# Kernel tuning notes

Hardware: AMD Instinct MI355X
Metric: run time of the kernel (lower is better)

The kernel has to match this reference:

```python
import jax, jax.numpy as jnp
import numpy as np

N_EMB = 1024
N_HEAD = 16
HD = N_EMB // N_HEAD
ROPE_BASE = 10000.0


def _rope_cos_sin(seq_len, dim, dtype):
    inv_freq = 1.0 / (ROPE_BASE ** (jnp.arange(0, dim, 2, dtype=jnp.float32) / dim))
    t = jnp.arange(seq_len, dtype=jnp.float32)
    freqs = jnp.outer(t, inv_freq)              # [S, dim/2]
    emb = jnp.concatenate([freqs, freqs], -1)    # [S, dim]
    return jnp.cos(emb).astype(dtype), jnp.sin(emb).astype(dtype)


def _rotate_half(x):
    x1, x2 = jnp.split(x, 2, axis=-1)
    return jnp.concatenate([-x2, x1], axis=-1)


def _apply_rope(x):
    # x: [B, H, L, hd]; rotary over sequence axis (-2)
    cos, sin = _rope_cos_sin(x.shape[-2], x.shape[-1], x.dtype)
    return x * cos + _rotate_half(x) * sin


def setup_inputs() -> dict:
    key = jax.random.key(0)
    ks = jax.random.split(key, 8)
    B, T, S = 2, 2048, 2048
    std = 0.02
    return {
        "x": jax.random.normal(ks[0], (B, T, N_EMB), jnp.float32),
        "memory": jax.random.normal(ks[1], (B, S, N_EMB), jnp.float32),
        "q_w": jax.random.normal(ks[2], (N_EMB, N_EMB), jnp.float32) * std,
        "q_b": jnp.zeros((N_EMB,), jnp.float32),
        "kv_w": jax.random.normal(ks[3], (N_EMB, 2 * N_EMB), jnp.float32) * std,
        "kv_b": jnp.zeros((2 * N_EMB,), jnp.float32),
        "proj_w": jax.random.normal(ks[4], (N_EMB, N_EMB), jnp.float32) * std,
        "proj_b": jnp.zeros((N_EMB,), jnp.float32),
    }


def reference(x, memory, q_w, q_b, kv_w, kv_b, proj_w, proj_b):
    B, S, C = memory.shape
    T = x.shape[1]
    kv = memory @ kv_w + kv_b                      # [B,S,2C]
    K, V = jnp.split(kv, 2, axis=-1)
    Q = x @ q_w + q_b                              # [B,T,C]

    def heads(t, L):
        return t.reshape(B, L, N_HEAD, HD).transpose(0, 2, 1, 3)

    Q, K, V = heads(Q, T), heads(K, S), heads(V, S)
    Q = jax.nn.elu(Q) + 1.0                        # positive feature map
    K = jax.nn.elu(K) + 1.0
    Q_rot = _apply_rope(Q)
    K_rot = _apply_rope(K)
    # denom row-sum: sum_s Q.K_s == Q . (sum_s K_s) -- identical math, no SxT matrix
    denom = jnp.einsum('bhtd,bhd->bht', Q, K.sum(axis=2))[..., None]  # [B,H,T,1]
    att = jnp.einsum('bhtd,bhsd->bhts', Q_rot, K_rot) / denom          # [B,H,T,S]
    y = jnp.einsum('bhts,bhsd->bhtd', att, V)                          # [B,H,T,hd]
    y = y.transpose(0, 2, 1, 3).reshape(B, T, C)
    return y @ proj_w + proj_b
```

## Files before the change

### kernel.cpp

```cpp
#include <hip/hip_runtime.h>
#include <cstddef>
#include <cstdint>

#define B_SZ  2
#define T_SEQ 2048
#define S_SEQ 2048
#define C_EMB 1024
#define NH    16
#define HD    64
#define KDIM  1024

typedef __attribute__((ext_vector_type(8))) short bf16x8;
typedef __attribute__((ext_vector_type(4))) float f32x4;

#define OFF_XH    ((size_t)0)
#define OFF_XL    ((size_t)2097152)
#define OFF_MEMH  ((size_t)4194304)
#define OFF_MEML  ((size_t)6291456)
#define OFF_QWH   ((size_t)8388608)
#define OFF_QWL   ((size_t)8912896)
#define OFF_KVWH  ((size_t)9437184)
#define OFF_KVWL  ((size_t)10485760)
#define OFF_PWH   ((size_t)11534336)
#define OFF_PWL   ((size_t)12058624)
#define OFF_KSUM  ((size_t)12582912)
#define OFF_MT    ((size_t)12584960)
#define OFF_TAB   ((size_t)12716032)
#define OFF_YH    ((size_t)12847104)
#define OFF_YL    ((size_t)14944256)
#define WS_FLOATS ((size_t)17041408)

__device__ __forceinline__ float elu1(float v) {
    return v > 0.0f ? v + 1.0f : __expf(v);
}
__device__ __forceinline__ unsigned short bf16_rne(float x) {
    union { float f; unsigned int u; } v; v.f = x;
    unsigned int u = v.u;
    return (unsigned short)((u + 0x7FFFu + ((u >> 16) & 1u)) >> 16);
}
__device__ __forceinline__ float bf16_to_f(unsigned short h) {
    union { unsigned int u; float f; } v; v.u = ((unsigned int)h) << 16;
    return v.f;
}

#define PREP_BLOCKS 13064

__device__ __forceinline__ void split4_body(
    const float4* __restrict__ in, ushort4* __restrict__ hi,
    ushort4* __restrict__ lo, int i)
{
    float4 v = in[i];
    ushort4 h, l;
    h.x = bf16_rne(v.x); l.x = bf16_rne(v.x - bf16_to_f(h.x));
    h.y = bf16_rne(v.y); l.y = bf16_rne(v.y - bf16_to_f(h.y));
    h.z = bf16_rne(v.z); l.z = bf16_rne(v.z - bf16_to_f(h.z));
    h.w = bf16_rne(v.w); l.w = bf16_rne(v.w - bf16_to_f(h.w));
    hi[i] = h; lo[i] = l;
}

__device__ __forceinline__ void transpose_body(
    const float* __restrict__ W, unsigned short* __restrict__ Wth,
    unsigned short* __restrict__ Wtl, int K, int N, int bx, int by,
    float (*tile)[33])
{
    const int k0 = by * 32, n0 = bx * 32;
    const int tx = threadIdx.x & 31, ty = threadIdx.x >> 5;
    #pragma unroll
    for (int j = 0; j < 4; ++j)
        tile[ty + j * 8][tx] = W[(size_t)(k0 + ty + j * 8) * N + n0 + tx];
    __syncthreads();
    #pragma unroll
    for (int j = 0; j < 4; ++j) {
        float x = tile[tx][ty + j * 8];
        unsigned short h = bf16_rne(x);
        unsigned short l = bf16_rne(x - bf16_to_f(h));
        size_t o = (size_t)(n0 + ty + j * 8) * K + k0 + tx;
        Wth[o] = h; Wtl[o] = l;
    }
}

__global__ __launch_bounds__(256) void prep_kernel(
    const float* __restrict__ x, const float* __restrict__ memory,
    const float* __restrict__ q_w, const float* __restrict__ kv_w,
    const float* __restrict__ proj_w,
    unsigned short* __restrict__ xh, unsigned short* __restrict__ xl,
    unsigned short* __restrict__ mh, unsigned short* __restrict__ ml,
    unsigned short* __restrict__ qwh, unsigned short* __restrict__ qwl,
    unsigned short* __restrict__ kvwh, unsigned short* __restrict__ kvwl,
    unsigned short* __restrict__ pwh, unsigned short* __restrict__ pwl,
    float2* __restrict__ tab, float* __restrict__ zero_base)
{
    __shared__ float tile[32][33];
    const int bid = blockIdx.x;
    const int tid = threadIdx.x;
    if (bid < 4096) {
        split4_body((const float4*)x, (ushort4*)xh, (ushort4*)xl, bid * 256 + tid);
    } else if (bid < 8192) {
        split4_body((const float4*)memory, (ushort4*)mh, (ushort4*)ml, (bid - 4096) * 256 + tid);
    } else if (bid < 9216) {
        int i = bid - 8192;
        transpose_body(q_w, qwh, qwl, 1024, 1024, i & 31, i >> 5, tile);
    } else if (bid < 11264) {
        int i = bid - 9216;
        transpose_body(kv_w, kvwh, kvwl, 1024, 2048, i & 63, i >> 6, tile);
    } else if (bid < 12288) {
        int i = bid - 11264;
        transpose_body(proj_w, pwh, pwl, 1024, 1024, i & 31, i >> 5, tile);
    } else if (bid < 12544) {
        int idx = (bid - 12288) * 256 + tid;
        int pos = idx >> 5, i = idx & 31;
        double invf = exp(-(double)i * (9.210340371976184 / 32.0));
        float arg = (float)((double)pos * invf);
        float sn, cs;
        sincosf(arg, &sn, &cs);
        tab[idx] = make_float2(cs, sn);
    } else {
        int idx = (bid - 12544) * 256 + tid;
        if (idx < 2048 + 131072) zero_base[idx] = 0.0f;
    }
}

__device__ __forceinline__ void gemm_main_loop_64(
    const unsigned short* __restrict__ Ah, const unsigned short* __restrict__ Al,
    const unsigned short* __restrict__ Bth, const unsigned short* __restrict__ Btl,
    unsigned short* lds, int m0, int n0, f32x4 acc[2][4])
{
    const int tid = threadIdx.x;
    const int w = tid >> 6, lane = tid & 63;
    const int quad = lane >> 4, lrow = lane & 15;
    const int srow = lane >> 2;
    const int scol = (lane & 3) * 8;

    const unsigned short* src = (w == 0) ? Ah : (w == 1) ? Al : (w == 2) ? Bth : Btl;
    const int rbase = (w < 2) ? m0 : n0;
    const unsigned short* gsrc = src + (size_t)(rbase + srow) * KDIM + scol;
    unsigned short* lbase = (w < 2) ? &lds[w * 8192] : &lds[16384 + (w - 2) * 4096];

    const unsigned short* As_h = lds;
    const unsigned short* As_l = lds + 8192;
    const unsigned short* Bs_h = lds + 16384;
    const unsigned short* Bs_l = lds + 20480;

    for (int k0 = 0; k0 < KDIM; k0 += 64) {
        if (w < 2) {
            #pragma unroll
            for (int p = 0; p < 2; ++p)
                #pragma unroll
                for (int i = 0; i < 8; ++i)
                    __builtin_amdgcn_global_load_lds(
                        (const __attribute__((address_space(1))) unsigned int*)(gsrc + (size_t)i * 16 * KDIM + k0 + p * 32),
                        (__attribute__((address_space(3))) unsigned int*)(lbase + p * 4096 + i * 512),
                        16, 0, 0);
        } else {
            #pragma unroll
            for (int p = 0; p < 2; ++p)
                #pragma unroll
                for (int i = 0; i < 4; ++i)
                    __builtin_amdgcn_global_load_lds(
                        (const __attribute__((address_space(1))) unsigned int*)(gsrc + (size_t)i * 16 * KDIM + k0 + p * 32),
                        (__attribute__((address_space(3))) unsigned int*)(lbase + p * 2048 + i * 512),
                        16, 0, 0);
        }
        __syncthreads();

        #pragma unroll
        for (int p = 0; p < 2; ++p) {
            bf16x8 bh[4], bl[4];
            #pragma unroll
            for (int jt = 0; jt < 4; ++jt) {
                int nl = jt * 16 + lrow;
                bh[jt] = *(const bf16x8*)&Bs_h[p * 2048 + nl * 32 + quad * 8];
                bl[jt] = *(const bf16x8*)&Bs_l[p * 2048 + nl * 32 + quad * 8];
            }
            #pragma unroll
            for (int it = 0; it < 2; ++it) {
                int ml = w * 32 + it * 16 + lrow;
                bf16x8 ah = *(const bf16x8*)&As_h[p * 4096 + ml * 32 + quad * 8];
                bf16x8 al = *(const bf16x8*)&As_l[p * 4096 + ml * 32 + quad * 8];
                #pragma unroll
                for (int jt = 0; jt < 4; ++jt) {
                    acc[it][jt] = __builtin_amdgcn_mfma_f32_16x16x32_bf16(ah, bh[jt], acc[it][jt], 0, 0, 0);
                    acc[it][jt] = __builtin_amdgcn_mfma_f32_16x16x32_bf16(ah, bl[jt], acc[it][jt], 0, 0, 0);
                    acc[it][jt] = __builtin_amdgcn_mfma_f32_16x16x32_bf16(al, bh[jt], acc[it][jt], 0, 0, 0);
                }
            }
        }
        __syncthreads();
    }
}

__global__ __launch_bounds__(256) void gemm_kv(
    const unsigned short* __restrict__ Ah, const unsigned short* __restrict__ Al,
    const unsigned short* __restrict__ Bth, const unsigned short* __restrict__ Btl,
    const float* __restrict__ bias, const float2* __restrict__ tab,
    float* __restrict__ Ksum, float* __restrict__ Mt)
{
    __shared__ unsigned short smem[34816];
    const int tid = threadIdx.x;
    const int w = tid >> 6, lane = tid & 63;
    const int wr = w >> 1, wc = w & 1;
    const int quad = lane >> 4, lrow = lane & 15;
    const int h  = blockIdx.x;
    const int m0 = blockIdx.y * 128;
    const int b  = m0 >> 11;
    const int tbase = (m0 & 2047) + wr * 64;

    {
        const unsigned short* src = (w == 0) ? Ah : (w == 1) ? Al : (w == 2) ? Bth : Btl;
        const int srow = lane >> 2, scol = (lane & 3) * 8;
        const size_t rowbase = (w < 2) ? (size_t)(m0 + srow) : (size_t)(h * 64 + srow);
        const unsigned short* gsrc = src + rowbase * KDIM + scol;
        const size_t vskip = (w >= 2) ? (size_t)960 * KDIM : 0;
        unsigned short* lbase = &smem[w * 8192];
        const unsigned short* As_h = smem;
        const unsigned short* As_l = smem + 8192;
        const unsigned short* Bs_h = smem + 16384;
        const unsigned short* Bs_l = smem + 24576;

        f32x4 acc[4][4] = {};
        for (int k0 = 0; k0 < KDIM; k0 += 64) {
            #pragma unroll
            for (int p = 0; p < 2; ++p)
                #pragma unroll
                for (int i = 0; i < 8; ++i) {
                    size_t goff = (size_t)i * 16 * KDIM + k0 + p * 32 + ((i >= 4) ? vskip : 0);
                    __builtin_amdgcn_global_load_lds(
                        (const __attribute__((address_space(1))) unsigned int*)(gsrc + goff),
                        (__attribute__((address_space(3))) unsigned int*)(lbase + p * 4096 + i * 512),
                        16, 0, 0);
                }
            __syncthreads();
            #pragma unroll
            for (int p = 0; p < 2; ++p) {
                bf16x8 bh[4], bl[4];
                #pragma unroll
                for (int jt = 0; jt < 4; ++jt) {
                    int nl = wc * 64 + jt * 16 + lrow;
                    bh[jt] = *(const bf16x8*)&Bs_h[p * 4096 + nl * 32 + quad * 8];
                    bl[jt] = *(const bf16x8*)&Bs_l[p * 4096 + nl * 32 + quad * 8];
                }
                #pragma unroll
                for (int it = 0; it < 4; ++it) {
                    int ml = wr * 64 + it * 16 + lrow;
                    bf16x8 ah = *(const bf16x8*)&As_h[p * 4096 + ml * 32 + quad * 8];
                    bf16x8 al = *(const bf16x8*)&As_l[p * 4096 + ml * 32 + quad * 8];
                    #pragma unroll
                    for (int jt = 0; jt < 4; ++jt) {
                        acc[it][jt] = __builtin_amdgcn_mfma_f32_16x16x32_bf16(ah, bh[jt], acc[it][jt], 0, 0, 0);
                        acc[it][jt] = __builtin_amdgcn_mfma_f32_16x16x32_bf16(ah, bl[jt], acc[it][jt], 0, 0, 0);
                        acc[it][jt] = __builtin_amdgcn_mfma_f32_16x16x32_bf16(al, bh[jt], acc[it][jt], 0, 0, 0);
                    }
                }
            }
            __syncthreads();
        }

        const bool isK = (wc == 0);
        const int colg = (isK ? 0 : C_EMB) + h * 64;
        float bb[4];
        #pragma unroll
        for (int jt = 0; jt < 4; ++jt) bb[jt] = bias[colg + jt * 16 + lrow];
        #pragma unroll
        for (int it = 0; it < 4; ++it)
            #pragma unroll
            for (int jt = 0; jt < 4; ++jt)
                #pragma unroll
                for (int r = 0; r < 4; ++r) {
                    float v = acc[it][jt][r] + bb[jt];
                    acc[it][jt][r] = isK ? elu1(v) : v;
                }

        if (isK) {
            #pragma unroll
            for (int jt = 0; jt < 4; ++jt) {
                float p = 0.0f;
                #pragma unroll
                for (int it = 0; it < 4; ++it)
                    #pragma unroll
                    for (int r = 0; r < 4; ++r) p += acc[it][jt][r];
                p += __shfl_xor(p, 16);
                p += __shfl_xor(p, 32);
                if (quad == 0)
                    atomicAdd(&Ksum[b * C_EMB + h * 64 + jt * 16 + lrow], p);
            }
            #pragma unroll
            for (int it = 0; it < 4; ++it)
                #pragma unroll
                for (int r = 0; r < 4; ++r) {
                    int s = tbase + it * 16 + quad * 4 + r;
                    float2 c0 = tab[s * 32 + lrow];
                    float2 c1 = tab[s * 32 + 16 + lrow];
                    float a0 = acc[it][0][r], a1 = acc[it][1][r];
                    float a2 = acc[it][2][r], a3 = acc[it][3][r];
                    acc[it][0][r] = a0 * c0.x - a2 * c0.y;
                    acc[it][2][r] = a2 * c0.x + a0 * c0.y;
                    acc[it][1][r] = a1 * c1.x - a3 * c1.y;
                    acc[it][3][r] = a3 * c1.x + a1 * c1.y;
                }
        }

        unsigned short* Hd = smem + (isK ? 0 : 17408);
        unsigned short* Ld = Hd + 8704;
        #pragma unroll
        for (int jt = 0; jt < 4; ++jt) {
            int d = jt * 16 + lrow;
            #pragma unroll
            for (int it = 0; it < 4; ++it) {
                int t0loc = wr * 64 + it * 16 + quad * 4;
                ushort4 h4, l4;
                float v0 = acc[it][jt][0], v1 = acc[it][jt][1];
                float v2 = acc[it][jt][2], v3 = acc[it][jt][3];
                h4.x = bf16_rne(v0); l4.x = bf16_rne(v0 - bf16_to_f(h4.x));
                h4.y = bf16_rne(v1); l4.y = bf16_rne(v1 - bf16_to_f(h4.y));
                h4.z = bf16_rne(v2); l4.z = bf16_rne(v2 - bf16_to_f(h4.z));
                h4.w = bf16_rne(v3); l4.w = bf16_rne(v3 - bf16_to_f(h4.w));
                *(ushort4*)&Hd[d * 136 + t0loc] = h4;
                *(ushort4*)&Ld[d * 136 + t0loc] = l4;
            }
        }
    }
    __syncthreads();

    {
        const unsigned short* KH = smem;
        const unsigned short* KL = smem + 8704;
        const unsigned short* VH = smem + 17408;
        const unsigned short* VL = smem + 26112;
        const int mrow = w * 16 + lrow;
        f32x4 macc[4] = {};
        #pragma unroll
        for (int ks = 0; ks < 4; ++ks) {
            int kof = ks * 32 + quad * 8;
            bf16x8 vah = *(const bf16x8*)&VH[mrow * 136 + kof];
            bf16x8 val = *(const bf16x8*)&VL[mrow * 136 + kof];
            #pragma unroll
            for (int jt = 0; jt < 4; ++jt) {
                int nrow = jt * 16 + lrow;
                bf16x8 kbh = *(const bf16x8*)&KH[nrow * 136 + kof];
                bf16x8 kbl = *(const bf16x8*)&KL[nrow * 136 + kof];
                macc[jt] = __builtin_amdgcn_mfma_f32_16x16x32_bf16(vah, kbh, macc[jt], 0, 0, 0);
                macc[jt] = __builtin_amdgcn_mfma_f32_16x16x32_bf16(vah, kbl, macc[jt], 0, 0, 0);
                macc[jt] = __builtin_amdgcn_mfma_f32_16x16x32_bf16(val, kbh, macc[jt], 0, 0, 0);
            }
        }
        const int bh = b * NH + h;
        #pragma unroll
        for (int jt = 0; jt < 4; ++jt)
            #pragma unroll
            for (int r = 0; r < 4; ++r)
                atomicAdd(&Mt[((size_t)bh * 64 + w * 16 + quad * 4 + r) * 64 + jt * 16 + lrow],
                          macc[jt][r]);
    }
}

__global__ __launch_bounds__(256) void gemm_q(
    const unsigned short* __restrict__ Ah, const unsigned short* __restrict__ Al,
    const unsigned short* __restrict__ Bth, const unsigned short* __restrict__ Btl,
    const float* __restrict__ bias, const float2* __restrict__ tab,
    const float* __restrict__ Ksum, const float* __restrict__ Mt,
    unsigned short* __restrict__ Yh, unsigned short* __restrict__ Yl)
{
    __shared__ unsigned short smem[24576];
    const int h  = blockIdx.x;
    const int m0 = blockIdx.y * 128;
    f32x4 acc[2][4] = {};
    gemm_main_loop_64(Ah, Al, Bth, Btl, smem, m0, h * 64, acc);

    const int tid = threadIdx.x;
    const int w = tid >> 6, lane = tid & 63;
    const int quad = lane >> 4, lrow = lane & 15;
    const int b = m0 >> 11;
    const int tbase = (m0 & 2047) + w * 32;
    const int bh = b * NH + h;

    float bb[4];
    #pragma unroll
    for (int jt = 0; jt < 4; ++jt) bb[jt] = bias[h * 64 + jt * 16 + lrow];
    #pragma unroll
    for (int it = 0; it < 2; ++it)
        #pragma unroll
        for (int jt = 0; jt < 4; ++jt)
            #pragma unroll
            for (int r = 0; r < 4; ++r)
                acc[it][jt][r] = elu1(acc[it][jt][r] + bb[jt]);

    float ks[4], den_reg[2][4];
    #pragma unroll
    for (int jt = 0; jt < 4; ++jt) ks[jt] = Ksum[b * C_EMB + h * 64 + jt * 16 + lrow];
    #pragma unroll
    for (int it = 0; it < 2; ++it)
        #pragma unroll
        for (int r = 0; r < 4; ++r) {
            float p = acc[it][0][r] * ks[0] + acc[it][1][r] * ks[1]
                    + acc[it][2][r] * ks[2] + acc[it][3][r] * ks[3];
            p += __shfl_xor(p, 1);
            p += __shfl_xor(p, 2);
            p += __shfl_xor(p, 4);
            p += __shfl_xor(p, 8);
            den_reg[it][r] = p;
        }

    #pragma unroll
    for (int it = 0; it < 2; ++it)
        #pragma unroll
        for (int r = 0; r < 4; ++r) {
            int s = tbase + it * 16 + quad * 4 + r;
            float2 c0 = tab[s * 32 + lrow];
            float2 c1 = tab[s * 32 + 16 + lrow];
            float a0 = acc[it][0][r], a1 = acc[it][1][r];
            float a2 = acc[it][2][r], a3 = acc[it][3][r];
            acc[it][0][r] = a0 * c0.x - a2 * c0.y;
            acc[it][2][r] = a2 * c0.x + a0 * c0.y;
            acc[it][1][r] = a1 * c1.x - a3 * c1.y;
            acc[it][3][r] = a3 * c1.x + a1 * c1.y;
        }

    unsigned short* QH = smem + w * 4608;
    unsigned short* QL = QH + 2304;
    #pragma unroll
    for (int it = 0; it < 2; ++it)
        #pragma unroll
        for (int jt = 0; jt < 4; ++jt)
            #pragma unroll
            for (int r = 0; r < 4; ++r) {
                int tloc = it * 16 + quad * 4 + r;
                int d = jt * 16 + lrow;
                float v = acc[it][jt][r];
                unsigned short hh = bf16_rne(v);
                QH[tloc * 72 + d] = hh;
                QL[tloc * 72 + d] = bf16_rne(v - bf16_to_f(hh));
            }

    f32x4 acc2[2][4] = {};
    #pragma unroll
    for (int kc = 0; kc < 2; ++kc) {
        bf16x8 mbh[4], mbl[4];
        #pragma unroll
        for (int jt2 = 0; jt2 < 4; ++jt2) {
            const float* mp = &Mt[((size_t)bh * 64 + jt2 * 16 + lrow) * 64 + kc * 32 + quad * 8];
            #pragma unroll
            for (int e = 0; e < 8; ++e) {
                float x = mp[e];
                unsigned short hh = bf16_rne(x);
                mbh[jt2][e] = (short)hh;
                mbl[jt2][e] = (short)bf16_rne(x - bf16_to_f(hh));
            }
        }
        #pragma unroll
        for (int it2 = 0; it2 < 2; ++it2) {
            int ro = (it2 * 16 + lrow) * 72 + kc * 32 + quad * 8;
            bf16x8 qh = *(const bf16x8*)&QH[ro];
            bf16x8 ql = *(const bf16x8*)&QL[ro];
            #pragma unroll
            for (int jt2 = 0; jt2 < 4; ++jt2) {
                acc2[it2][jt2] = __builtin_amdgcn_mfma_f32_16x16x32_bf16(qh, mbh[jt2], acc2[it2][jt2], 0, 0, 0);
                acc2[it2][jt2] = __builtin_amdgcn_mfma_f32_16x16x32_bf16(qh, mbl[jt2], acc2[it2][jt2], 0, 0, 0);
                acc2[it2][jt2] = __builtin_amdgcn_mfma_f32_16x16x32_bf16(ql, mbh[jt2], acc2[it2][jt2], 0, 0, 0);
            }
        }
    }

    #pragma unroll
    for (int it2 = 0; it2 < 2; ++it2)
        #pragma unroll
        for (int jt2 = 0; jt2 < 4; ++jt2)
            #pragma unroll
            for (int r = 0; r < 4; ++r) {
                float v = acc2[it2][jt2][r] / den_reg[it2][r];
                size_t o = ((size_t)(m0 + w * 32 + it2 * 16 + quad * 4 + r)) * C_EMB
                         + h * 64 + jt2 * 16 + lrow;
                unsigned short hh = bf16_rne(v);
                Yh[o] = hh;
                Yl[o] = bf16_rne(v - bf16_to_f(hh));
            }
}

__global__ __launch_bounds__(256) void gemm_out(
    const unsigned short* __restrict__ Ah, const unsigned short* __restrict__ Al,
    const unsigned short* __restrict__ Bth, const unsigned short* __restrict__ Btl,
    const float* __restrict__ bias, float* __restrict__ out)
{
    __shared__ unsigned short lds[24576];
    const int m0 = blockIdx.y * 128, n0 = blockIdx.x * 64;
    f32x4 acc[2][4] = {};
    gemm_main_loop_64(Ah, Al, Bth, Btl, lds, m0, n0, acc);

    const int tid = threadIdx.x;
    const int w = tid >> 6, lane = tid & 63;
    const int quad = lane >> 4, lrow = lane & 15;

    #pragma unroll
    for (int jt = 0; jt < 4; ++jt) {
        int gc = n0 + jt * 16 + lrow;
        float bb = bias[gc];
        #pragma unroll
        for (int it = 0; it < 2; ++it) {
            int grb = m0 + w * 32 + it * 16 + quad * 4;
            #pragma unroll
            for (int r = 0; r < 4; ++r)
                out[(size_t)(grb + r) * C_EMB + gc] = acc[it][jt][r] + bb;
        }
    }
}

extern "C" void kernel_launch(void* const* d_in, const int* in_sizes, int n_in,
                              void* d_out, int out_size, void* d_ws, size_t ws_size,
                              hipStream_t stream)
{
    const float* x      = (const float*)d_in[0];
    const float* memory = (const float*)d_in[1];
    const float* q_w    = (const float*)d_in[2];
    const float* q_b    = (const float*)d_in[3];
    const float* kv_w   = (const float*)d_in[4];
    const float* kv_b   = (const float*)d_in[5];
    const float* proj_w = (const float*)d_in[6];
    const float* proj_b = (const float*)d_in[7];

    if (ws_size < WS_FLOATS * sizeof(float)) return;

    float* ws = (float*)d_ws;
    unsigned short* xh   = (unsigned short*)(ws + OFF_XH);
    unsigned short* xl   = (unsigned short*)(ws + OFF_XL);
    unsigned short* mh   = (unsigned short*)(ws + OFF_MEMH);
    unsigned short* ml   = (unsigned short*)(ws + OFF_MEML);
    unsigned short* qwh  = (unsigned short*)(ws + OFF_QWH);
    unsigned short* qwl  = (unsigned short*)(ws + OFF_QWL);
    unsigned short* kvwh = (unsigned short*)(ws + OFF_KVWH);
    unsigned short* kvwl = (unsigned short*)(ws + OFF_KVWL);
    unsigned short* pwh  = (unsigned short*)(ws + OFF_PWH);
    unsigned short* pwl  = (unsigned short*)(ws + OFF_PWL);
    unsigned short* Yh   = (unsigned short*)(ws + OFF_YH);
    unsigned short* Yl   = (unsigned short*)(ws + OFF_YL);
    float*  Ksum = ws + OFF_KSUM;
    float*  Mm   = ws + OFF_MT;
    float2* tab  = (float2*)(ws + OFF_TAB);

    prep_kernel<<<PREP_BLOCKS, 256, 0, stream>>>(
        x, memory, q_w, kv_w, proj_w,
        xh, xl, mh, ml, qwh, qwl, kvwh, kvwl, pwh, pwl,
        tab, Ksum );

    gemm_kv<<<dim3(16, 32), 256, 0, stream>>>(mh, ml, kvwh, kvwl, kv_b, tab, Ksum, Mm);
    gemm_q<<<dim3(16, 32), 256, 0, stream>>>(xh, xl, qwh, qwl, q_b, tab, Ksum, Mm, Yh, Yl);
    gemm_out<<<dim3(16, 32), 256, 0, stream>>>(Yh, Yl, pwh, pwl, proj_b, (float*)d_out);
}
```

Measured before the change: 245.2 us.

## Triple-buffer GEMM main loop with async LDS loads and larger 256-row tiles

Replaces the single-buffered GEMM loop with a templated pipeline that keeps three LDS buffers in flight. It prefetches two k-steps ahead with global_load_lds, waits with explicit vmcnt counts, applies an XOR swizzle to LDS, and raises MFMA priority with setprio. Blocks grow to 512 threads and 256 rows, halving the grid, and the KV epilogue LDS layout is resized to match. The aim is to hide global-load latency and cut barrier stalls; the cost is more LDS per block, lower occupancy and fewer blocks to spread across CUs.

Result: faster. 234.5 us (-4.4%).

```diff
diff --git a/kernel.cpp b/kernel.cpp
--- a/kernel.cpp
+++ b/kernel.cpp
@@ -120,251 +120,276 @@
     }
 }
 
-__device__ __forceinline__ void gemm_main_loop_64(
+#define WAITCNT_VM(N) asm volatile("s_waitcnt vmcnt(" #N ")" ::: "memory")
+#define WAIT_LGKM0()  asm volatile("s_waitcnt lgkmcnt(0)" ::: "memory")
+
+template<int BN, int M_IT, bool KV>
+__device__ __forceinline__ void gemm_pipe(
     const unsigned short* __restrict__ Ah, const unsigned short* __restrict__ Al,
     const unsigned short* __restrict__ Bth, const unsigned short* __restrict__ Btl,
-    unsigned short* lds, int m0, int n0, f32x4 acc[2][4])
-{
+    unsigned short* lds, int m0, int n0, f32x4 (&acc)[M_IT][4])
+{
+    constexpr int BUFSZ = 16384 + 2 * BN * 32;
+    constexpr int NT = KDIM / 32;
     const int tid = threadIdx.x;
     const int w = tid >> 6, lane = tid & 63;
     const int quad = lane >> 4, lrow = lane & 15;
-    const int srow = lane >> 2;
-    const int scol = (lane & 3) * 8;
-
-    const unsigned short* src = (w == 0) ? Ah : (w == 1) ? Al : (w == 2) ? Bth : Btl;
-    const int rbase = (w < 2) ? m0 : n0;
-    const unsigned short* gsrc = src + (size_t)(rbase + srow) * KDIM + scol;
-    unsigned short* lbase = (w < 2) ? &lds[w * 8192] : &lds[16384 + (w - 2) * 4096];
-
-    const unsigned short* As_h = lds;
-    const unsigned short* As_l = lds + 8192;
-    const unsigned short* Bs_h = lds + 16384;
-    const unsigned short* Bs_l = lds + 20480;
-
-    for (int k0 = 0; k0 < KDIM; k0 += 64) {
-        if (w < 2) {
-            #pragma unroll
-            for (int p = 0; p < 2; ++p)
-                #pragma unroll
-                for (int i = 0; i < 8; ++i)
-                    __builtin_amdgcn_global_load_lds(
-                        (const __attribute__((address_space(1))) unsigned int*)(gsrc + (size_t)i * 16 * KDIM + k0 + p * 32),
-                        (__attribute__((address_space(3))) unsigned int*)(lbase + p * 4096 + i * 512),
-                        16, 0, 0);
+    const int sr = tid >> 2;
+    const int g  = (tid & 3) ^ ((tid >> 3) & 3);
+    constexpr int WAVES_N = (BN == 128) ? 2 : 1;
+    const int wr = (WAVES_N == 2) ? (w >> 1) : w;
+    const int wc = (WAVES_N == 2) ? (w & 1) : 0;
+    const int rowbase = wr * (M_IT * 16);
+    const int colbase = wc * 64;
+    const int sw = ((quad ^ ((lrow >> 1) & 3)) << 3);
+
+    const unsigned short* gA0 = Ah + (size_t)(m0 + sr) * KDIM + g * 8;
+    const unsigned short* gA1 = Ah + (size_t)(m0 + 128 + sr) * KDIM + g * 8;
+    const unsigned short* gA2 = Al + (size_t)(m0 + sr) * KDIM + g * 8;
+    const unsigned short* gA3 = Al + (size_t)(m0 + 128 + sr) * KDIM + g * 8;
+    const unsigned short* gB0;
+    const unsigned short* gB1 = nullptr;
+    if constexpr (KV) {
+        size_t brow = (size_t)(n0 + sr) + (sr >= 64 ? (size_t)960 : 0);
+        gB0 = Bth + brow * KDIM + g * 8;
+        gB1 = Btl + brow * KDIM + g * 8;
+    } else {
+        const unsigned short* bsrc = (w < 4) ? Bth : Btl;
+        gB0 = bsrc + (size_t)(n0 + (sr & 63)) * KDIM + g * 8;
+    }
+    const int lA0 = w * 512;
+    const int lA1 = 4096 + w * 512;
+    const int lA2 = 8192 + w * 512;
+    const int lA3 = 12288 + w * 512;
+    int lB0, lB1 = 0;
+    if constexpr (KV) {
+        lB0 = 16384 + w * 512;
+        lB1 = 20480 + w * 512;
+    } else {
+        lB0 = 16384 + ((w >= 4) ? 2048 : 0) + (w & 3) * 512;
+    }
+
+    auto STAGE = [&](unsigned short* buf, int k0) {
+        __builtin_amdgcn_global_load_lds(
+            (const __attribute__((address_space(1))) unsigned int*)(gA0 + k0),
+            (__attribute__((address_space(3))) unsigned int*)(buf + lA0), 16, 0, 0);
+        __builtin_amdgcn_global_load_lds(
+            (const __attribute__((address_space(1))) unsigned int*)(gA1 + k0),
+            (__attribute__((address_space(3))) unsigned int*)(buf + lA1), 16, 0, 0);
+        __builtin_amdgcn_global_load_lds(
+            (const __attribute__((address_space(1))) unsigned int*)(gA2 + k0),
+            (__attribute__((address_space(3))) unsigned int*)(buf + lA2), 16, 0, 0);
+        __builtin_amdgcn_global_load_lds(
+            (const __attribute__((address_space(1))) unsigned int*)(gA3 + k0),
+            (__attribute__((address_space(3))) unsigned int*)(buf + lA3), 16, 0, 0);
+        __builtin_amdgcn_global_load_lds(
+            (const __attribute__((address_space(1))) unsigned int*)(gB0 + k0),
+            (__attribute__((address_space(3))) unsigned int*)(buf + lB0), 16, 0, 0);
+        if constexpr (KV)
+            __builtin_amdgcn_global_load_lds(
+                (const __attribute__((address_space(1))) unsigned int*)(gB1 + k0),
+                (__attribute__((address_space(3))) unsigned int*)(buf + lB1), 16, 0, 0);
+    };
+
+    unsigned short* cur = lds;
+    unsigned short* nxt = lds + BUFSZ;
+    unsigned short* thr = lds + 2 * BUFSZ;
+    STAGE(cur, 0);
+    STAGE(nxt, 32);
+
+    #pragma unroll 1
+    for (int t = 0; t < NT; ++t) {
+        if (t == NT - 1) {
+            WAITCNT_VM(0);
         } else {
-            #pragma unroll
-            for (int p = 0; p < 2; ++p)
-                #pragma unroll
-                for (int i = 0; i < 4; ++i)
-                    __builtin_amdgcn_global_load_lds(
-                        (const __attribute__((address_space(1))) unsigned int*)(gsrc + (size_t)i * 16 * KDIM + k0 + p * 32),
-                        (__attribute__((address_space(3))) unsigned int*)(lbase + p * 2048 + i * 512),
-                        16, 0, 0);
-        }
-        __syncthreads();
-
-        #pragma unroll
-        for (int p = 0; p < 2; ++p) {
-            bf16x8 bh[4], bl[4];
-            #pragma unroll
-            for (int jt = 0; jt < 4; ++jt) {
-                int nl = jt * 16 + lrow;
-                bh[jt] = *(const bf16x8*)&Bs_h[p * 2048 + nl * 32 + quad * 8];
-                bl[jt] = *(const bf16x8*)&Bs_l[p * 2048 + nl * 32 + quad * 8];
-            }
-            #pragma unroll
-            for (int it = 0; it < 2; ++it) {
-                int ml = w * 32 + it * 16 + lrow;
-                bf16x8 ah = *(const bf16x8*)&As_h[p * 4096 + ml * 32 + quad * 8];
-                bf16x8 al = *(const bf16x8*)&As_l[p * 4096 + ml * 32 + quad * 8];
-                #pragma unroll
-                for (int jt = 0; jt < 4; ++jt) {
-                    acc[it][jt] = __builtin_amdgcn_mfma_f32_16x16x32_bf16(ah, bh[jt], acc[it][jt], 0, 0, 0);
-                    acc[it][jt] = __builtin_amdgcn_mfma_f32_16x16x32_bf16(ah, bl[jt], acc[it][jt], 0, 0, 0);
-                    acc[it][jt] = __builtin_amdgcn_mfma_f32_16x16x32_bf16(al, bh[jt], acc[it][jt], 0, 0, 0);
-                }
-            }
-        }
-        __syncthreads();
-    }
-}
-
-__global__ __launch_bounds__(256) void gemm_kv(
+            if constexpr (KV) { WAITCNT_VM(6); } else { WAITCNT_VM(5); }
+        }
+        __builtin_amdgcn_s_barrier();
+
+        bf16x8 ah[M_IT], al[M_IT];
+        #pragma unroll
+        for (int it = 0; it < M_IT; ++it) {
+            int off = (rowbase + it * 16 + lrow) * 32 + sw;
+            ah[it] = *(const bf16x8*)&cur[off];
+            al[it] = *(const bf16x8*)&cur[8192 + off];
+        }
+        bf16x8 bh[2], bl[2];
+        #pragma unroll
+        for (int jt = 0; jt < 2; ++jt) {
+            int boff = (colbase + jt * 16 + lrow) * 32 + sw;
+            bh[jt] = *(const bf16x8*)&cur[16384 + boff];
+            bl[jt] = *(const bf16x8*)&cur[16384 + BN * 32 + boff];
+        }
+        if (t + 2 < NT) STAGE(thr, (t + 2) * 32);
+        __builtin_amdgcn_s_barrier();
+        WAIT_LGKM0();
+        __builtin_amdgcn_sched_barrier(0);
+        __builtin_amdgcn_s_setprio(1);
+        #pragma unroll
+        for (int it = 0; it < M_IT; ++it)
+            #pragma unroll
+            for (int jt = 0; jt < 2; ++jt) {
+                acc[it][jt] = __builtin_amdgcn_mfma_f32_16x16x32_bf16(ah[it], bh[jt], acc[it][jt], 0, 0, 0);
+                acc[it][jt] = __builtin_amdgcn_mfma_f32_16x16x32_bf16(ah[it], bl[jt], acc[it][jt], 0, 0, 0);
+                acc[it][jt] = __builtin_amdgcn_mfma_f32_16x16x32_bf16(al[it], bh[jt], acc[it][jt], 0, 0, 0);
+            }
+        __builtin_amdgcn_s_setprio(0);
+        __builtin_amdgcn_s_barrier();
+
+        #pragma unroll
+        for (int jt = 0; jt < 2; ++jt) {
+            int boff = (colbase + (jt + 2) * 16 + lrow) * 32 + sw;
+            bh[jt] = *(const bf16x8*)&cur[16384 + boff];
+            bl[jt] = *(const bf16x8*)&cur[16384 + BN * 32 + boff];
+        }
+        __builtin_amdgcn_s_barrier();
+        WAIT_LGKM0();
+        __builtin_amdgcn_sched_barrier(0);
+        __builtin_amdgcn_s_setprio(1);
+        #pragma unroll
+        for (int it = 0; it < M_IT; ++it)
+            #pragma unroll
+            for (int jt = 0; jt < 2; ++jt) {
+                acc[it][jt + 2] = __builtin_amdgcn_mfma_f32_16x16x32_bf16(ah[it], bh[jt], acc[it][jt + 2], 0, 0, 0);
+                acc[it][jt + 2] = __builtin_amdgcn_mfma_f32_16x16x32_bf16(ah[it], bl[jt], acc[it][jt + 2], 0, 0, 0);
+                acc[it][jt + 2] = __builtin_amdgcn_mfma_f32_16x16x32_bf16(al[it], bh[jt], acc[it][jt + 2], 0, 0, 0);
+            }
+        __builtin_amdgcn_s_setprio(0);
+
+        unsigned short* tmp = cur; cur = nxt; nxt = thr; thr = tmp;
+    }
+    __syncthreads();
+}
+
+__global__ __launch_bounds__(512) void gemm_kv(
     const unsigned short* __restrict__ Ah, const unsigned short* __restrict__ Al,
     const unsigned short* __restrict__ Bth, const unsigned short* __restrict__ Btl,
     const float* __restrict__ bias, const float2* __restrict__ tab,
     float* __restrict__ Ksum, float* __restrict__ Mt)
 {
-    __shared__ unsigned short smem[34816];
+    __shared__ alignas(16) unsigned short smem[73728];
     const int tid = threadIdx.x;
     const int w = tid >> 6, lane = tid & 63;
     const int wr = w >> 1, wc = w & 1;
     const int quad = lane >> 4, lrow = lane & 15;
     const int h  = blockIdx.x;
-    const int m0 = blockIdx.y * 128;
+    const int m0 = blockIdx.y * 256;
     const int b  = m0 >> 11;
     const int tbase = (m0 & 2047) + wr * 64;
-
-    {
-        const unsigned short* src = (w == 0) ? Ah : (w == 1) ? Al : (w == 2) ? Bth : Btl;
-        const int srow = lane >> 2, scol = (lane & 3) * 8;
-        const size_t rowbase = (w < 2) ? (size_t)(m0 + srow) : (size_t)(h * 64 + srow);
-        const unsigned short* gsrc = src + rowbase * KDIM + scol;
-        const size_t vskip = (w >= 2) ? (size_t)960 * KDIM : 0;
-        unsigned short* lbase = &smem[w * 8192];
-        const unsigned short* As_h = smem;
-        const unsigned short* As_l = smem + 8192;
-        const unsigned short* Bs_h = smem + 16384;
-        const unsigned short* Bs_l = smem + 24576;
-
-        f32x4 acc[4][4] = {};
-        for (int k0 = 0; k0 < KDIM; k0 += 64) {
-            #pragma unroll
-            for (int p = 0; p < 2; ++p)
-                #pragma unroll
-                for (int i = 0; i < 8; ++i) {
-                    size_t goff = (size_t)i * 16 * KDIM + k0 + p * 32 + ((i >= 4) ? vskip : 0);
-                    __builtin_amdgcn_global_load_lds(
-                        (const __attribute__((address_space(1))) unsigned int*)(gsrc + goff),
-                        (__attribute__((address_space(3))) unsigned int*)(lbase + p * 4096 + i * 512),
-                        16, 0, 0);
-                }
-            __syncthreads();
-            #pragma unroll
-            for (int p = 0; p < 2; ++p) {
-                bf16x8 bh[4], bl[4];
-                #pragma unroll
-                for (int jt = 0; jt < 4; ++jt) {
-                    int nl = wc * 64 + jt * 16 + lrow;
-                    bh[jt] = *(const bf16x8*)&Bs_h[p * 4096 + nl * 32 + quad * 8];
-                    bl[jt] = *(const bf16x8*)&Bs_l[p * 4096 + nl * 32 + quad * 8];
-                }
-                #pragma unroll
-                for (int it = 0; it < 4; ++it) {
-                    int ml = wr * 64 + it * 16 + lrow;
-                    bf16x8 ah = *(const bf16x8*)&As_h[p * 4096 + ml * 32 + quad * 8];
-                    bf16x8 al = *(const bf16x8*)&As_l[p * 4096 + ml * 32 + quad * 8];
-                    #pragma unroll
-                    for (int jt = 0; jt < 4; ++jt) {
-                        acc[it][jt] = __builtin_amdgcn_mfma_f32_16x16x32_bf16(ah, bh[jt], acc[it][jt], 0, 0, 0);
-                        acc[it][jt] = __builtin_amdgcn_mfma_f32_16x16x32_bf16(ah, bl[jt], acc[it][jt], 0, 0, 0);
-                        acc[it][jt] = __builtin_amdgcn_mfma_f32_16x16x32_bf16(al, bh[jt], acc[it][jt], 0, 0, 0);
-                    }
-                }
-            }
-            __syncthreads();
-        }
-
-        const bool isK = (wc == 0);
-        const int colg = (isK ? 0 : C_EMB) + h * 64;
-        float bb[4];
-        #pragma unroll
-        for (int jt = 0; jt < 4; ++jt) bb[jt] = bias[colg + jt * 16 + lrow];
-        #pragma unroll
-        for (int it = 0; it < 4; ++it)
-            #pragma unroll
-            for (int jt = 0; jt < 4; ++jt)
-                #pragma unroll
-                for (int r = 0; r < 4; ++r) {
-                    float v = acc[it][jt][r] + bb[jt];
-                    acc[it][jt][r] = isK ? elu1(v) : v;
-                }
-
-        if (isK) {
-            #pragma unroll
-            for (int jt = 0; jt < 4; ++jt) {
-                float p = 0.0f;
-                #pragma unroll
-                for (int it = 0; it < 4; ++it)
-                    #pragma unroll
-                    for (int r = 0; r < 4; ++r) p += acc[it][jt][r];
-                p += __shfl_xor(p, 16);
-                p += __shfl_xor(p, 32);
-                if (quad == 0)
-                    atomicAdd(&Ksum[b * C_EMB + h * 64 + jt * 16 + lrow], p);
-            }
+    const int bh_idx = b * NH + h;
+
+    f32x4 acc[4][4] = {};
+    gemm_pipe<128, 4, true>(Ah, Al, Bth, Btl, smem, m0, h * 64, acc);
+
+    const bool isK = (wc == 0);
+    const int colg = (isK ? 0 : C_EMB) + h * 64;
+    float bb[4];
+    #pragma unroll
+    for (int jt = 0; jt < 4; ++jt) bb[jt] = bias[colg + jt * 16 + lrow];
+    #pragma unroll
+    for (int it = 0; it < 4; ++it)
+        #pragma unroll
+        for (int jt = 0; jt < 4; ++jt)
+            #pragma unroll
+            for (int r = 0; r < 4; ++r) {
+                float v = acc[it][jt][r] + bb[jt];
+                acc[it][jt][r] = isK ? elu1(v) : v;
+            }
+
+    if (isK) {
+        #pragma unroll
+        for (int jt = 0; jt < 4; ++jt) {
+            float p = 0.0f;
             #pragma unroll
             for (int it = 0; it < 4; ++it)
                 #pragma unroll
-                for (int r = 0; r < 4; ++r) {
-                    int s = tbase + it * 16 + quad * 4 + r;
-                    float2 c0 = tab[s * 32 + lrow];
-                    float2 c1 = tab[s * 32 + 16 + lrow];
-                    float a0 = acc[it][0][r], a1 = acc[it][1][r];
-                    float a2 = acc[it][2][r], a3 = acc[it][3][r];
-                    acc[it][0][r] = a0 * c0.x - a2 * c0.y;
-                    acc[it][2][r] = a2 * c0.x + a0 * c0.y;
-                    acc[it][1][r] = a1 * c1.x - a3 * c1.y;
-                    acc[it][3][r] = a3 * c1.x + a1 * c1.y;
-                }
-        }
-
-        unsigned short* Hd = smem + (isK ? 0 : 17408);
-        unsigned short* Ld = Hd + 8704;
-        #pragma unroll
-        for (int jt = 0; jt < 4; ++jt) {
-            int d = jt * 16 + lrow;
-            #pragma unroll
-            for (int it = 0; it < 4; ++it) {
-                int t0loc = wr * 64 + it * 16 + quad * 4;
-                ushort4 h4, l4;
-                float v0 = acc[it][jt][0], v1 = acc[it][jt][1];
-                float v2 = acc[it][jt][2], v3 = acc[it][jt][3];
-                h4.x = bf16_rne(v0); l4.x = bf16_rne(v0 - bf16_to_f(h4.x));
-                h4.y = bf16_rne(v1); l4.y = bf16_rne(v1 - bf16_to_f(h4.y));
-                h4.z = bf16_rne(v2); l4.z = bf16_rne(v2 - bf16_to_f(h4.z));
-                h4.w = bf16_rne(v3); l4.w = bf16_rne(v3 - bf16_to_f(h4.w));
-                *(ushort4*)&Hd[d * 136 + t0loc] = h4;
-                *(ushort4*)&Ld[d * 136 + t0loc] = l4;
-            }
+                for (int r = 0; r < 4; ++r) p += acc[it][jt][r];
+            p += __shfl_xor(p, 16);
+            p += __shfl_xor(p, 32);
+            if (quad == 0)
+                atomicAdd(&Ksum[b * C_EMB + h * 64 + jt * 16 + lrow], p);
+        }
+        #pragma unroll
+        for (int it = 0; it < 4; ++it)
+            #pragma unroll
+            for (int r = 0; r < 4; ++r) {
+                int s = tbase + it * 16 + quad * 4 + r;
+                float2 c0 = tab[s * 32 + lrow];
+                float2 c1 = tab[s * 32 + 16 + lrow];
+                float a0 = acc[it][0][r], a1 = acc[it][1][r];
+                float a2 = acc[it][2][r], a3 = acc[it][3][r];
+                acc[it][0][r] = a0 * c0.x - a2 * c0.y;
+                acc[it][2][r] = a2 * c0.x + a0 * c0.y;
+                acc[it][1][r] = a1 * c1.x - a3 * c1.y;
+                acc[it][3][r] = a3 * c1.x + a1 * c1.y;
+            }
+    }
+
+    unsigned short* Hd = smem + (isK ? 0 : 33792);
+    unsigned short* Ld = Hd + 16896;
+    #pragma unroll
+    for (int jt = 0; jt < 4; ++jt) {
+        int d = jt * 16 + lrow;
+        #pragma unroll
+        for (int it = 0; it < 4; ++it) {
+            int t0loc = wr * 64 + it * 16 + quad * 4;
+            ushort4 h4, l4;
+            float v0 = acc[it][jt][0], v1 = acc[it][jt][1];
+            float v2 = acc[it][jt][2], v3 = acc[it][jt][3];
+            h4.x = bf16_rne(v0); l4.x = bf16_rne(v0 - bf16_to_f(h4.x));
+            h4.y = bf16_rne(v1); l4.y = bf16_rne(v1 - bf16_to_f(h4.y));
+            h4.z = bf16_rne(v2); l4.z = bf16_rne(v2 - bf16_to_f(h4.z));
+            h4.w = bf16_rne(v3); l4.w = bf16_rne(v3 - bf16_to_f(h4.w));
+            *(ushort4*)&Hd[d * 264 + t0loc] = h4;
+            *(ushort4*)&Ld[d * 264 + t0loc] = l4;
         }
     }
     __syncthreads();
 
     {
         const unsigned short* KH = smem;
-        const unsigned short* KL = smem + 8704;
-        const unsigned short* VH = smem + 17408;
-        const unsigned short* VL = smem + 26112;
-        const int mrow = w * 16 + lrow;
+        const unsigned short* KL = smem + 16896;
+        const unsigned short* VH = smem + 33792;
+        const unsigned short* VL = smem + 50688;
+        const int mrow = (w & 3) * 16 + lrow;
+        const int thalf = w >> 2;
         f32x4 macc[4] = {};
         #pragma unroll
         for (int ks = 0; ks < 4; ++ks) {
-            int kof = ks * 32 + quad * 8;
-            bf16x8 vah = *(const bf16x8*)&VH[mrow * 136 + kof];
-            bf16x8 val = *(const bf16x8*)&VL[mrow * 136 + kof];
+            int kof = thalf * 128 + ks * 32 + quad * 8;
+            bf16x8 vah = *(const bf16x8*)&VH[mrow * 264 + kof];
+            bf16x8 val = *(const bf16x8*)&VL[mrow * 264 + kof];
             #pragma unroll
             for (int jt = 0; jt < 4; ++jt) {
                 int nrow = jt * 16 + lrow;
-                bf16x8 kbh = *(const bf16x8*)&KH[nrow * 136 + kof];
-                bf16x8 kbl = *(const bf16x8*)&KL[nrow * 136 + kof];
+                bf16x8 kbh = *(const bf16x8*)&KH[nrow * 264 + kof];
+                bf16x8 kbl = *(const bf16x8*)&KL[nrow * 264 + kof];
                 macc[jt] = __builtin_amdgcn_mfma_f32_16x16x32_bf16(vah, kbh, macc[jt], 0, 0, 0);
                 macc[jt] = __builtin_amdgcn_mfma_f32_16x16x32_bf16(vah, kbl, macc[jt], 0, 0, 0);
                 macc[jt] = __builtin_amdgcn_mfma_f32_16x16x32_bf16(val, kbh, macc[jt], 0, 0, 0);
             }
         }
-        const int bh = b * NH + h;
         #pragma unroll
         for (int jt = 0; jt < 4; ++jt)
             #pragma unroll
             for (int r = 0; r < 4; ++r)
-                atomicAdd(&Mt[((size_t)bh * 64 + w * 16 + quad * 4 + r) * 64 + jt * 16 + lrow],
+                atomicAdd(&Mt[((size_t)bh_idx * 64 + (w & 3) * 16 + quad * 4 + r) * 64 + jt * 16 + lrow],
                           macc[jt][r]);
     }
 }
 
-__global__ __launch_bounds__(256) void gemm_q(
+__global__ __launch_bounds__(512) void gemm_q(
     const unsigned short* __restrict__ Ah, const unsigned short* __restrict__ Al,
     const unsigned short* __restrict__ Bth, const unsigned short* __restrict__ Btl,
     const float* __restrict__ bias, const float2* __restrict__ tab,
     const float* __restrict__ Ksum, const float* __restrict__ Mt,
     unsigned short* __restrict__ Yh, unsigned short* __restrict__ Yl)
 {
-    __shared__ unsigned short smem[24576];
+    __shared__ alignas(16) unsigned short smem[61440];
     const int h  = blockIdx.x;
-    const int m0 = blockIdx.y * 128;
+    const int m0 = blockIdx.y * 256;
     f32x4 acc[2][4] = {};
-    gemm_main_loop_64(Ah, Al, Bth, Btl, smem, m0, h * 64, acc);
+    gemm_pipe<64, 2, false>(Ah, Al, Bth, Btl, smem, m0, h * 64, acc);
 
     const int tid = threadIdx.x;
     const int w = tid >> 6, lane = tid & 63;
@@ -475,15 +500,15 @@
             }
 }
 
-__global__ __launch_bounds__(256) void gemm_out(
+__global__ __launch_bounds__(512) void gemm_out(
     const unsigned short* __restrict__ Ah, const unsigned short* __restrict__ Al,
     const unsigned short* __restrict__ Bth, const unsigned short* __restrict__ Btl,
     const float* __restrict__ bias, float* __restrict__ out)
 {
-    __shared__ unsigned short lds[24576];
-    const int m0 = blockIdx.y * 128, n0 = blockIdx.x * 64;
+    __shared__ alignas(16) unsigned short smem[61440];
+    const int m0 = blockIdx.y * 256, n0 = blockIdx.x * 64;
     f32x4 acc[2][4] = {};
-    gemm_main_loop_64(Ah, Al, Bth, Btl, lds, m0, n0, acc);
+    gemm_pipe<64, 2, false>(Ah, Al, Bth, Btl, smem, m0, n0, acc);
 
     const int tid = threadIdx.x;
     const int w = tid >> 6, lane = tid & 63;
@@ -540,7 +565,7 @@
         xh, xl, mh, ml, qwh, qwl, kvwh, kvwl, pwh, pwl,
         tab, Ksum );
 
-    gemm_kv<<<dim3(16, 32), 256, 0, stream>>>(mh, ml, kvwh, kvwl, kv_b, tab, Ksum, Mm);
-    gemm_q<<<dim3(16, 32), 256, 0, stream>>>(xh, xl, qwh, qwl, q_b, tab, Ksum, Mm, Yh, Yl);
-    gemm_out<<<dim3(16, 32), 256, 0, stream>>>(Yh, Yl, pwh, pwl, proj_b, (float*)d_out);
-}
+    gemm_kv<<<dim3(16, 16), 512, 0, stream>>>(mh, ml, kvwh, kvwl, kv_b, tab, Ksum, Mm);
+    gemm_q<<<dim3(16, 16), 512, 0, stream>>>(xh, xl, qwh, qwl, q_b, tab, Ksum, Mm, Yh, Yl);
+    gemm_out<<<dim3(16, 16), 512, 0, stream>>>(Yh, Yl, pwh, pwl, proj_b, (float*)d_out);
+}
```
